# Optimization experiments

Hardware: AMD Instinct MI355X
Metric: run time of the kernel (lower is better)

## Reference

```python
import jax, jax.numpy as jnp
import numpy as np

# theta (Kruschke-style ALCOVE hyperparameters, from init_kwargs)
RHO = 2.0
TAU = 1.0
BETA = 6.5
GAMMA = 0.0
PHI = 2.0
LAM_A = 0.001
LAM_W = 0.003

B, D, H, O = 256, 64, 2048, 32  # batch, n_dim, n_hidden, n_output


def setup_inputs() -> dict:
    key = jax.random.key(0)
    k1, k2, k3, k4, k5 = jax.random.split(key, 5)
    z = jax.random.normal(k1, (B, D), dtype=jnp.float32)
    labels = jax.random.randint(k2, (B,), 0, O)
    one_hot_label = jax.nn.one_hot(labels, O, dtype=jnp.float32)
    attention = jax.random.uniform(k3, (B, D), dtype=jnp.float32)
    association = 0.05 * jax.random.normal(k4, (B, H, O), dtype=jnp.float32)
    coordinates = jax.random.normal(k5, (H, D), dtype=jnp.float32)
    return {
        'z': z,
        'one_hot_label': one_hot_label,
        'attention': attention,
        'association': association,
        'coordinates': coordinates,
    }


def reference(z, one_hot_label, attention, association, coordinates):
    """One ALCOVECell RNN step: RBF similarity -> readout -> ALCOVE loss ->
    analytic state update via autodiff. Returns (x_out_scaled, new_attention, new_association)."""

    def loss_fn(att, assoc):
        # weighted Minkowski distance: (B, H)
        diff = jnp.abs(z[:, None, :] - coordinates[None, :, :]) ** RHO  # (B, H, D)
        d = jnp.sum(diff * att[:, None, :], axis=-1) ** (1.0 / RHO)
        # RBF similarity and readout
        s = jnp.exp(-BETA * d ** TAU) + GAMMA                            # (B, H)
        x_out = jnp.einsum('bh,bho->bo', s, assoc)                       # (B, O)
        # ALCOVE humble-teacher loss (gradients flow through teacher, as in TF)
        t_min = jnp.minimum(-1.0, x_out)
        teacher = t_min - one_hot_label * t_min
        t_max = jnp.maximum(1.0, x_out)
        teacher = teacher + one_hot_label * t_max
        loss = jnp.mean(jnp.square(teacher - x_out), axis=1)             # (B,)
        # TF tape.gradient on a vector loss sums over batch
        return jnp.sum(loss), x_out

    (dl_da, dl_dw), x_out = jax.grad(loss_fn, argnums=(0, 1), has_aux=True)(
        attention, association)

    x_out_scaled = PHI * x_out
    new_attention = jnp.maximum(attention - LAM_A * dl_da, 0.0)
    new_association = association - LAM_W * dl_dw
    return x_out_scaled, new_attention, new_association
```

## Files before the change

kernel.cpp:

```cpp
#include <hip/hip_runtime.h>
#include <math.h>


#define BB 256
#define DD 64
#define HH 2048
#define OO 32
#define NSL 8
#define HS (HH / NSL)
#define BETA 6.5f
#define PHI 2.0f
#define LAM_A 0.001f
#define LAM_W 0.003f
#define NT 256

__global__ __launch_bounds__(NT) void k0_transpose(
    const float* __restrict__ coords, float* __restrict__ ct)
{
    int idx = blockIdx.x * NT + threadIdx.x;
    int d = idx >> 11;
    int h = idx & (HH - 1);
    ct[idx] = coords[h * DD + d];
}

__global__ __launch_bounds__(NT) void k1_sim(
    const float* __restrict__ z,
    const float* __restrict__ att,
    const float* __restrict__ assoc,
    const float* __restrict__ ct,
    float* __restrict__ s_all,
    float* __restrict__ r_all,
    float* __restrict__ px)
{
    __shared__ float2 za[DD];
    __shared__ float s_loc[HS];
    __shared__ float red[NT * 4];

    const int b  = blockIdx.x >> 3;
    const int sl = blockIdx.x & 7;
    const int base = sl * HS;
    const int t = threadIdx.x;
    const int h = base + t;

    if (t < DD)
        za[t] = make_float2(z[b * DD + t], att[b * DD + t]);
    __syncthreads();

    float S = 0.0f;
    const float* ctp = ct + h;
    #pragma unroll 8
    for (int d = 0; d < DD; ++d) {
        float2 p = za[d];
        float c = ctp[d * HH];
        float diff = p.x - c;
        S = fmaf(p.y * diff, diff, S);
    }
    S = S < 0.0f ? 0.0f : S;
    float dd = sqrtf(S);
    float sh = expf(-BETA * dd);
    s_all[b * HH + h] = sh;
    r_all[b * HH + h] = (dd > 0.0f) ? (-BETA * sh / (2.0f * dd)) : 0.0f;
    s_loc[t] = sh;
    __syncthreads();

    const int o4 = t & 7;
    const int hl = t >> 3;
    const float4* assoc4 = (const float4*)(assoc + (size_t)b * HH * OO);

    float4 acc = make_float4(0.f, 0.f, 0.f, 0.f);
    #pragma unroll
    for (int chunk = 0; chunk < HS / 32; ++chunk) {
        int hloc = chunk * 32 + hl;
        float s2 = s_loc[hloc];
        float4 a = assoc4[(base + hloc) * (OO / 4) + o4];
        acc.x = fmaf(s2, a.x, acc.x);
        acc.y = fmaf(s2, a.y, acc.y);
        acc.z = fmaf(s2, a.z, acc.z);
        acc.w = fmaf(s2, a.w, acc.w);
    }
    ((float4*)red)[t] = acc;
    __syncthreads();

    if (t < OO) {
        const int b4 = t >> 2, comp = t & 3;
        float x = 0.0f;
        #pragma unroll 8
        for (int g = 0; g < 32; ++g)
            x += red[(g * 8 + b4) * 4 + comp];
        px[(b * NSL + sl) * OO + t] = x;
    }
}

__global__ __launch_bounds__(NT) void k2_upd(
    const float* __restrict__ z,
    const float* __restrict__ one_hot,
    const float* __restrict__ assoc,
    const float* __restrict__ coords,
    const float* __restrict__ s_all,
    const float* __restrict__ r_all,
    const float* __restrict__ px,
    float* __restrict__ gatt_part,
    float* __restrict__ out)
{
    __shared__ float gx_s[OO];
    __shared__ float s_loc[HS];
    __shared__ float r_loc[HS];
    __shared__ float coeff[HS];
    __shared__ float red[NT];

    const int b  = blockIdx.x >> 3;
    const int sl = blockIdx.x & 7;
    const int base = sl * HS;
    const int t = threadIdx.x;
    const int lane = t & 63;
    const int wave = t >> 6;

    if (t < OO) {
        float x = 0.0f;
        #pragma unroll
        for (int s2 = 0; s2 < NSL; ++s2)
            x += px[(b * NSL + s2) * OO + t];
        float oh = one_hot[b * OO + t];
        float tmin = fminf(-1.0f, x);
        float tmax = fmaxf(1.0f, x);
        float teacher = tmin - oh * tmin + oh * tmax;
        gx_s[t] = (2.0f / OO) * (x - teacher);
        if (sl == 0)
            out[b * OO + t] = PHI * x;
    }
    s_loc[t] = s_all[b * HH + base + t];
    r_loc[t] = r_all[b * HH + base + t];
    __syncthreads();

    const int o4 = t & 7;
    const int hl = t >> 3;
    const float4 gxv = ((const float4*)gx_s)[o4];
    const float4* assoc4 = (const float4*)(assoc + (size_t)b * HH * OO);
    float4* out_assoc4 = (float4*)(out + BB * OO + BB * DD) + (size_t)b * HH * (OO / 4);

    #pragma unroll
    for (int chunk = 0; chunk < HS / 32; ++chunk) {
        int hloc = chunk * 32 + hl;
        float sh = s_loc[hloc];
        float4 a = assoc4[(base + hloc) * (OO / 4) + o4];
        float w = LAM_W * sh;
        float4 na;
        na.x = fmaf(-w, gxv.x, a.x);
        na.y = fmaf(-w, gxv.y, a.y);
        na.z = fmaf(-w, gxv.z, a.z);
        na.w = fmaf(-w, gxv.w, a.w);
        out_assoc4[(base + hloc) * (OO / 4) + o4] = na;

        float part = a.x * gxv.x + a.y * gxv.y + a.z * gxv.z + a.w * gxv.w;
        part += __shfl_xor(part, 1, 64);
        part += __shfl_xor(part, 2, 64);
        part += __shfl_xor(part, 4, 64);
        if (o4 == 0)
            coeff[hloc] = r_loc[hloc] * part;
    }
    __syncthreads();

    const float zd = z[b * DD + lane];
    float acc = 0.0f;
    #pragma unroll 4
    for (int i = 0; i < 64; ++i) {
        int hloc = wave * 64 + i;
        float cf = coeff[hloc];
        float c = coords[(base + hloc) * DD + lane];
        float diff = zd - c;
        acc = fmaf(cf * diff, diff, acc);
    }
    red[t] = acc;
    __syncthreads();

    if (t < DD) {
        float g = red[t] + red[64 + t] + red[128 + t] + red[192 + t];
        gatt_part[(b * NSL + sl) * DD + t] = g;
    }
}

__global__ __launch_bounds__(NT) void k3_att(
    const float* __restrict__ att,
    const float* __restrict__ gatt_part,
    float* __restrict__ out)
{
    int idx = blockIdx.x * NT + threadIdx.x;
    int b = idx >> 6;
    int d = idx & 63;
    float g = 0.0f;
    #pragma unroll
    for (int sl = 0; sl < NSL; ++sl)
        g += gatt_part[(b * NSL + sl) * DD + d];
    float na = att[b * DD + d] - LAM_A * g;
    out[BB * OO + idx] = na > 0.0f ? na : 0.0f;
}

extern "C" void kernel_launch(void* const* d_in, const int* in_sizes, int n_in,
                              void* d_out, int out_size, void* d_ws, size_t ws_size,
                              hipStream_t stream) {
    const float* z       = (const float*)d_in[0];
    const float* one_hot = (const float*)d_in[1];
    const float* att     = (const float*)d_in[2];
    const float* assoc   = (const float*)d_in[3];
    const float* coords  = (const float*)d_in[4];
    float* out = (float*)d_out;

    float* ws = (float*)d_ws;
    float* ct        = ws;
    float* s_all     = ct + DD * HH;
    float* r_all     = s_all + BB * HH;
    float* px        = r_all + BB * HH;
    float* gatt_part = px + BB * NSL * OO;

    k0_transpose<<<dim3((DD * HH) / NT), dim3(NT), 0, stream>>>(coords, ct);
    k1_sim<<<dim3(BB * NSL), dim3(NT), 0, stream>>>(z, att, assoc, ct,
                                                    s_all, r_all, px);
    k2_upd<<<dim3(BB * NSL), dim3(NT), 0, stream>>>(z, one_hot, assoc, coords,
                                                    s_all, r_all, px, gatt_part, out);
    k3_att<<<dim3((BB * DD) / NT), dim3(NT), 0, stream>>>(att, gatt_part, out);
}
```

Measured before the change: 143.3 us.

## Fuse similarity, update and attention kernels into one cooperative grid-synced kernel

Merges the three per-step kernels into one cooperative kernel with grid-wide syncs. The similarity values and their derivative factors now stay in shared memory instead of round-tripping through workspace buffers, and two kernel launches go away. The hidden dimension is split into 4 slices per batch row instead of 8, giving 1024 blocks that must all be co-resident for the cooperative launch. The grid syncs add their own cost, and occupancy limits could make the launch fail.

New measurement: 371.4 us. 159% more time.

```diff
diff --git a/kernel.cpp b/kernel.cpp
--- a/kernel.cpp
+++ b/kernel.cpp
@@ -1,13 +1,16 @@
 #include <hip/hip_runtime.h>
+#include <hip/hip_cooperative_groups.h>
 #include <math.h>
+
+namespace cg = cooperative_groups;
 
 
 #define BB 256
 #define DD 64
 #define HH 2048
 #define OO 32
-#define NSL 8
-#define HS (HH / NSL)
+#define NP 4
+#define HP (HH / NP)
 #define BETA 6.5f
 #define PHI 2.0f
 #define LAM_A 0.001f
@@ -23,44 +26,50 @@
     ct[idx] = coords[h * DD + d];
 }
 
-__global__ __launch_bounds__(NT) void k1_sim(
+__global__ __launch_bounds__(NT, 4) void k_fused(
     const float* __restrict__ z,
+    const float* __restrict__ one_hot,
     const float* __restrict__ att,
     const float* __restrict__ assoc,
+    const float* __restrict__ coords,
     const float* __restrict__ ct,
-    float* __restrict__ s_all,
-    float* __restrict__ r_all,
-    float* __restrict__ px)
+    float* __restrict__ px,
+    float* __restrict__ gatt_part,
+    float* __restrict__ out)
 {
     __shared__ float2 za[DD];
-    __shared__ float s_loc[HS];
-    __shared__ float red[NT * 4];
-
-    const int b  = blockIdx.x >> 3;
-    const int sl = blockIdx.x & 7;
-    const int base = sl * HS;
-    const int t = threadIdx.x;
-    const int h = base + t;
+    __shared__ float  s_loc[HP];
+    __shared__ float  rc_loc[HP];
+    __shared__ float4 red4[NT];
+    __shared__ float  gx_s[OO];
+
+    const int b    = blockIdx.x >> 2;
+    const int p    = blockIdx.x & 3;
+    const int base = p * HP;
+    const int t    = threadIdx.x;
 
     if (t < DD)
         za[t] = make_float2(z[b * DD + t], att[b * DD + t]);
     __syncthreads();
 
-    float S = 0.0f;
-    const float* ctp = ct + h;
-    #pragma unroll 8
-    for (int d = 0; d < DD; ++d) {
-        float2 p = za[d];
-        float c = ctp[d * HH];
-        float diff = p.x - c;
-        S = fmaf(p.y * diff, diff, S);
-    }
-    S = S < 0.0f ? 0.0f : S;
-    float dd = sqrtf(S);
-    float sh = expf(-BETA * dd);
-    s_all[b * HH + h] = sh;
-    r_all[b * HH + h] = (dd > 0.0f) ? (-BETA * sh / (2.0f * dd)) : 0.0f;
-    s_loc[t] = sh;
+    #pragma unroll
+    for (int ss = 0; ss < 2; ++ss) {
+        const int h = base + ss * NT + t;
+        float S = 0.0f;
+        const float* ctp = ct + h;
+        #pragma unroll 8
+        for (int d = 0; d < DD; ++d) {
+            float2 pz = za[d];
+            float c = ctp[d * HH];
+            float diff = pz.x - c;
+            S = fmaf(pz.y * diff, diff, S);
+        }
+        S = S < 0.0f ? 0.0f : S;
+        float dd = sqrtf(S);
+        float sh = expf(-BETA * dd);
+        s_loc[ss * NT + t]  = sh;
+        rc_loc[ss * NT + t] = (dd > 0.0f) ? (-BETA * sh / (2.0f * dd)) : 0.0f;
+    }
     __syncthreads();
 
     const int o4 = t & 7;
@@ -68,8 +77,8 @@
     const float4* assoc4 = (const float4*)(assoc + (size_t)b * HH * OO);
 
     float4 acc = make_float4(0.f, 0.f, 0.f, 0.f);
-    #pragma unroll
-    for (int chunk = 0; chunk < HS / 32; ++chunk) {
+    #pragma unroll 4
+    for (int chunk = 0; chunk < HP / 32; ++chunk) {
         int hloc = chunk * 32 + hl;
         float s2 = s_loc[hloc];
         float4 a = assoc4[(base + hloc) * (OO / 4) + o4];
@@ -78,68 +87,41 @@
         acc.z = fmaf(s2, a.z, acc.z);
         acc.w = fmaf(s2, a.w, acc.w);
     }
-    ((float4*)red)[t] = acc;
+    red4[t] = acc;
     __syncthreads();
 
     if (t < OO) {
+        const float* red = (const float*)red4;
         const int b4 = t >> 2, comp = t & 3;
         float x = 0.0f;
         #pragma unroll 8
         for (int g = 0; g < 32; ++g)
             x += red[(g * 8 + b4) * 4 + comp];
-        px[(b * NSL + sl) * OO + t] = x;
-    }
-}
-
-__global__ __launch_bounds__(NT) void k2_upd(
-    const float* __restrict__ z,
-    const float* __restrict__ one_hot,
-    const float* __restrict__ assoc,
-    const float* __restrict__ coords,
-    const float* __restrict__ s_all,
-    const float* __restrict__ r_all,
-    const float* __restrict__ px,
-    float* __restrict__ gatt_part,
-    float* __restrict__ out)
-{
-    __shared__ float gx_s[OO];
-    __shared__ float s_loc[HS];
-    __shared__ float r_loc[HS];
-    __shared__ float coeff[HS];
-    __shared__ float red[NT];
-
-    const int b  = blockIdx.x >> 3;
-    const int sl = blockIdx.x & 7;
-    const int base = sl * HS;
-    const int t = threadIdx.x;
-    const int lane = t & 63;
-    const int wave = t >> 6;
+        px[(b * NP + p) * OO + t] = x;
+    }
+
+    cg::this_grid().sync();
 
     if (t < OO) {
         float x = 0.0f;
         #pragma unroll
-        for (int s2 = 0; s2 < NSL; ++s2)
-            x += px[(b * NSL + s2) * OO + t];
+        for (int q = 0; q < NP; ++q)
+            x += px[(b * NP + q) * OO + t];
         float oh = one_hot[b * OO + t];
         float tmin = fminf(-1.0f, x);
         float tmax = fmaxf(1.0f, x);
         float teacher = tmin - oh * tmin + oh * tmax;
         gx_s[t] = (2.0f / OO) * (x - teacher);
-        if (sl == 0)
+        if (p == 0)
             out[b * OO + t] = PHI * x;
     }
-    s_loc[t] = s_all[b * HH + base + t];
-    r_loc[t] = r_all[b * HH + base + t];
-    __syncthreads();
-
-    const int o4 = t & 7;
-    const int hl = t >> 3;
+    __syncthreads();
+
     const float4 gxv = ((const float4*)gx_s)[o4];
-    const float4* assoc4 = (const float4*)(assoc + (size_t)b * HH * OO);
     float4* out_assoc4 = (float4*)(out + BB * OO + BB * DD) + (size_t)b * HH * (OO / 4);
 
-    #pragma unroll
-    for (int chunk = 0; chunk < HS / 32; ++chunk) {
+    #pragma unroll 4
+    for (int chunk = 0; chunk < HP / 32; ++chunk) {
         int hloc = chunk * 32 + hl;
         float sh = s_loc[hloc];
         float4 a = assoc4[(base + hloc) * (OO / 4) + o4];
@@ -156,43 +138,44 @@
         part += __shfl_xor(part, 2, 64);
         part += __shfl_xor(part, 4, 64);
         if (o4 == 0)
-            coeff[hloc] = r_loc[hloc] * part;
-    }
-    __syncthreads();
-
-    const float zd = z[b * DD + lane];
-    float acc = 0.0f;
-    #pragma unroll 4
-    for (int i = 0; i < 64; ++i) {
-        int hloc = wave * 64 + i;
-        float cf = coeff[hloc];
-        float c = coords[(base + hloc) * DD + lane];
-        float diff = zd - c;
-        acc = fmaf(cf * diff, diff, acc);
-    }
-    red[t] = acc;
-    __syncthreads();
-
+            rc_loc[hloc] *= part;
+    }
+    __syncthreads();
+
+    {
+        const int lane = t & 63, wave = t >> 6;
+        const float zd = za[lane].x;
+        float* red = (float*)red4;
+        float ga = 0.0f;
+        #pragma unroll 4
+        for (int i = 0; i < HP / 4; ++i) {
+            int hloc = wave * (HP / 4) + i;
+            float cf = rc_loc[hloc];
+            float c = coords[(size_t)(base + hloc) * DD + lane];
+            float diff = zd - c;
+            ga = fmaf(cf * diff, diff, ga);
+        }
+        red[t] = ga;
+    }
+    __syncthreads();
     if (t < DD) {
+        const float* red = (const float*)red4;
         float g = red[t] + red[64 + t] + red[128 + t] + red[192 + t];
-        gatt_part[(b * NSL + sl) * DD + t] = g;
-    }
-}
-
-__global__ __launch_bounds__(NT) void k3_att(
-    const float* __restrict__ att,
-    const float* __restrict__ gatt_part,
-    float* __restrict__ out)
-{
-    int idx = blockIdx.x * NT + threadIdx.x;
-    int b = idx >> 6;
-    int d = idx & 63;
-    float g = 0.0f;
-    #pragma unroll
-    for (int sl = 0; sl < NSL; ++sl)
-        g += gatt_part[(b * NSL + sl) * DD + d];
-    float na = att[b * DD + d] - LAM_A * g;
-    out[BB * OO + idx] = na > 0.0f ? na : 0.0f;
+        gatt_part[(b * NP + p) * DD + t] = g;
+    }
+
+    cg::this_grid().sync();
+
+    if (blockIdx.x < (BB * DD) / NT) {
+        int idx = blockIdx.x * NT + t;
+        int bb = idx >> 6, d = idx & 63;
+        float g = 0.0f;
+        #pragma unroll
+        for (int q = 0; q < NP; ++q)
+            g += gatt_part[(bb * NP + q) * DD + d];
+        float na = att[bb * DD + d] - LAM_A * g;
+        out[BB * OO + idx] = na > 0.0f ? na : 0.0f;
+    }
 }
 
 extern "C" void kernel_launch(void* const* d_in, const int* in_sizes, int n_in,
@@ -207,15 +190,14 @@
 
     float* ws = (float*)d_ws;
     float* ct        = ws;
-    float* s_all     = ct + DD * HH;
-    float* r_all     = s_all + BB * HH;
-    float* px        = r_all + BB * HH;
-    float* gatt_part = px + BB * NSL * OO;
+    float* px        = ct + DD * HH;
+    float* gatt_part = px + BB * NP * OO;
 
     k0_transpose<<<dim3((DD * HH) / NT), dim3(NT), 0, stream>>>(coords, ct);
-    k1_sim<<<dim3(BB * NSL), dim3(NT), 0, stream>>>(z, att, assoc, ct,
-                                                    s_all, r_all, px);
-    k2_upd<<<dim3(BB * NSL), dim3(NT), 0, stream>>>(z, one_hot, assoc, coords,
-                                                    s_all, r_all, px, gatt_part, out);
-    k3_att<<<dim3((BB * DD) / NT), dim3(NT), 0, stream>>>(att, gatt_part, out);
+
+    void* args[] = { (void*)&z, (void*)&one_hot, (void*)&att, (void*)&assoc,
+                     (void*)&coords, (void*)&ct, (void*)&px, (void*)&gatt_part,
+                     (void*)&out };
+    hipLaunchCooperativeKernel((const void*)k_fused, dim3(BB * NP), dim3(NT),
+                               args, 0, stream);
 }
```
